# Kernel tuning notes

Measured on AMD Instinct MI355X. Metric: run time of the kernel, lower is better.

Reference implementation:

```python
import jax, jax.numpy as jnp
import numpy as np

H_HEADS = 8
EPS = 1e-5

def layernorm(x, g, b):
    m = jnp.mean(x, axis=-1, keepdims=True)
    v = jnp.mean(jnp.square(x - m), axis=-1, keepdims=True)
    return (x - m) * jax.lax.rsqrt(v + EPS) * g + b

def setup_inputs() -> dict:
    key = jax.random.key(0)
    ks = jax.random.split(key, 8)
    B, H, W, C = 8, 64, 64, 256
    C2 = 2 * C
    s = lambda n: 1.0 / np.sqrt(n)
    return {
        "x1": jax.random.normal(ks[0], (B, H, W, C), jnp.float32),
        "x2": jax.random.normal(ks[1], (B, H, W, C), jnp.float32),
        "norm1_g": jnp.ones((C,)), "norm1_b": jnp.zeros((C,)),
        "lin_w": jax.random.normal(ks[2], (C, C), jnp.float32) * s(C),
        "lin_b": jnp.zeros((C,)),
        "reproj_w": jax.random.normal(ks[3], (C, C), jnp.float32) * s(C),
        "reproj_b": jnp.zeros((C,)),
        "attn_norm_g": jnp.ones((C,)), "attn_norm_b": jnp.zeros((C,)),
        "norm2_g": jnp.ones((C,)), "norm2_b": jnp.zeros((C,)),
        "fc1_w": jax.random.normal(ks[4], (C2, C), jnp.float32) * s(C),
        "fc1_b": jnp.zeros((C2,)),
        "dw_w": jax.random.normal(ks[5], (C2, 1, 3, 3), jnp.float32) * s(9),
        "dw_b": jnp.zeros((C2,)),
        "ffn_n1_g": jnp.ones((C2,)), "ffn_n1_b": jnp.zeros((C2,)),
        "fc2_w": jax.random.normal(ks[6], (C, C2), jnp.float32) * s(C2),
        "fc2_b": jnp.zeros((C,)),
        "ffn_n3_g": jnp.ones((C,)), "ffn_n3_b": jnp.zeros((C,)),
    }

def reference(x1, x2, norm1_g, norm1_b, lin_w, lin_b, reproj_w, reproj_b,
              attn_norm_g, attn_norm_b, norm2_g, norm2_b, fc1_w, fc1_b,
              dw_w, dw_b, ffn_n1_g, ffn_n1_b, fc2_w, fc2_b, ffn_n3_g, ffn_n3_b):
    B, H, W, C = x1.shape
    N = H * W
    h = H_HEADS
    dk = C // h  # head key channels; value_dim == key_dim == C here
    # shared norm1 + linear projection of both streams
    n1 = layernorm(x1, norm1_g, norm1_b) @ lin_w.T + lin_b  # (B,H,W,C) queries src
    n2 = layernorm(x2, norm1_g, norm1_b) @ lin_w.T + lin_b  # (B,H,W,C) key/value src
    # (B,N,C) -> (B,h,d,N); channel dim split contiguously per head (matches torch slicing)
    q = jnp.transpose(n1.reshape(B, N, h, dk), (0, 2, 3, 1))
    k = jnp.transpose(n2.reshape(B, N, h, dk), (0, 2, 3, 1))
    v = k  # values are the same tensor slices (value_dim == key_dim)
    k = jax.nn.softmax(k, axis=-1)   # softmax over tokens N
    q = jax.nn.softmax(q, axis=2)    # softmax over head channel dim
    # linear attention: context (B,h,dk,dv), then project back to tokens
    context = jnp.einsum('bhdn,bhvn->bhdv', k, v)
    att = jnp.einsum('bhdv,bhdn->bhvn', context, q)  # (B,h,dv,N)
    agg = att.reshape(B, C, H, W)
    # 1x1 conv reprojection (value_channels -> key_channels)
    rep = jnp.einsum('bvhw,kv->bhwk', agg, reproj_w) + reproj_b  # (B,H,W,C)
    attn_out = layernorm(rep, attn_norm_g, attn_norm_b)
    # out_proj is Identity since key_dim == in_dim
    tx = attn_out + x1
    y = layernorm(tx, norm2_g, norm2_b)  # skip_ffn input
    # skip_ffn
    h1 = y @ fc1_w.T + fc1_b  # (B,H,W,2C)
    hc = jnp.transpose(h1, (0, 3, 1, 2))  # NCHW
    dw = jax.lax.conv_general_dilated(
        hc, dw_w, window_strides=(1, 1), padding='SAME',
        dimension_numbers=('NCHW', 'OIHW', 'NCHW'),
        feature_group_count=hc.shape[1])
    dw = jnp.transpose(dw + dw_b[None, :, None, None], (0, 2, 3, 1))  # NHWC
    ax = jax.nn.gelu(layernorm(dw, ffn_n1_g, ffn_n1_b), approximate=False)
    out = ax @ fc2_w.T + fc2_b
    return layernorm(out + y, ffn_n3_g, ffn_n3_b)
```

## Files before the change

### kernel.cpp

```cpp
#include <hip/hip_runtime.h>

#define BTOK 32768
#define CC 256
#define CC2 512
#define NBATCH 8

typedef __bf16 bf16x8 __attribute__((ext_vector_type(8)));
typedef float f32x4 __attribute__((ext_vector_type(4)));
typedef unsigned short u16x8 __attribute__((ext_vector_type(8)));
typedef unsigned short u16x4 __attribute__((ext_vector_type(4)));

__device__ __forceinline__ float b2f(unsigned short u) {
    return __uint_as_float(((unsigned)u) << 16);
}
__device__ __forceinline__ unsigned short f2b(float f) {
    unsigned x = __float_as_uint(f);
    return (unsigned short)((x + 0x7fffu + ((x >> 16) & 1u)) >> 16);
}
__device__ __forceinline__ float wredsum(float v) {
#pragma unroll
    for (int m = 1; m < 64; m <<= 1) v += __shfl_xor(v, m);
    return v;
}
__device__ __forceinline__ float grp4sum(float v) {
    v += __shfl_xor(v, 1);
    v += __shfl_xor(v, 2);
    return v;
}

typedef __attribute__((address_space(3))) unsigned int lds_u32;
typedef const __attribute__((address_space(1))) unsigned int glb_u32;
__device__ __forceinline__ void gload_lds16(const unsigned short* g, unsigned short* l) {
    __builtin_amdgcn_global_load_lds((glb_u32*)g, (lds_u32*)l, 16, 0, 0);
}

__global__ __launch_bounds__(256) void probe_kernel(
    const unsigned short* __restrict__ x, int* __restrict__ flag)
{
    int t = threadIdx.x;
    int c = 0;
    for (int i = t; i < 1024; i += 256) {
        unsigned e = (x[i] >> 7) & 0xFFu;
        c += (e >= 110u && e <= 135u) ? 1 : 0;
    }
#pragma unroll
    for (int m = 1; m < 64; m <<= 1) c += __shfl_xor(c, m);
    __shared__ int acc[4];
    if ((t & 63) == 0) acc[t >> 6] = c;
    __syncthreads();
    if (t == 0) *flag = ((acc[0] + acc[1] + acc[2] + acc[3]) >= 896) ? 1 : 0;
}

__global__ __launch_bounds__(256) void cvt_params_kernel(
    const int* __restrict__ flagp,
    const void* p0, const void* p1, const void* p2, const void* p3, const void* p4,
    const void* p5, const void* p6, const void* p7, const void* p8, const void* p9,
    const void* p10, const void* p11, const void* p12, const void* p13, const void* p14,
    const void* p15, const void* p16, const void* p17, const void* p18, const void* p19,
    unsigned short* __restrict__ dst)
{
    bool isb = (*flagp != 0);
    long g = (long)blockIdx.x * 256 + threadIdx.x;
    long str = (long)gridDim.x * 256;
#define CVT(src, off, n)                                                        \
    for (long i = g; i < (long)(n); i += str)                                   \
        dst[(off) + i] = isb ? ((const unsigned short*)(src))[i]                \
                             : f2b(((const float*)(src))[i]);
    CVT(p0, 0, 256)
    CVT(p1, 256, 256)
    CVT(p2, 512, 65536)
    CVT(p3, 66048, 256)
    CVT(p4, 66304, 65536)
    CVT(p5, 131840, 256)
    CVT(p6, 132096, 256)
    CVT(p7, 132352, 256)
    CVT(p8, 132608, 256)
    CVT(p9, 132864, 256)
    CVT(p10, 133120, 131072)
    CVT(p11, 264192, 512)
    CVT(p12, 264704, 4608)
    CVT(p13, 269312, 512)
    CVT(p14, 269824, 512)
    CVT(p15, 270336, 512)
    CVT(p16, 270848, 131072)
    CVT(p17, 401920, 256)
    CVT(p18, 402176, 256)
    CVT(p19, 402432, 256)
#undef CVT
}

__global__ __launch_bounds__(256) void dw_transpose_kernel(
    const void* __restrict__ src, unsigned short* __restrict__ dwt,
    const int* __restrict__ flagp)
{
    bool isb = (*flagp != 0);
    for (int i = threadIdx.x; i < 4608; i += 256) {
        int tap = i >> 9, c = i & 511;
        dwt[i] = isb ? ((const unsigned short*)src)[c * 9 + tap]
                     : f2b(((const float*)src)[c * 9 + tap]);
    }
}

__global__ __launch_bounds__(256) void ln_dual_kernel(
    const void* __restrict__ x1, const void* __restrict__ x2,
    const unsigned short* __restrict__ g, const unsigned short* __restrict__ b,
    unsigned short* __restrict__ out, const int* __restrict__ flagp)
{
    bool isb = (*flagp != 0);
    int wid = threadIdx.x >> 6, l = threadIdx.x & 63;
    long row = (long)blockIdx.x * 4 + wid;
    const void* xsel = (row < BTOK) ? x1 : x2;
    long r = (row < BTOK) ? row : (row - BTOK);
    float f[4];
    if (isb) {
        u16x4 v = *reinterpret_cast<const u16x4*>((const unsigned short*)xsel + r * CC + l * 4);
#pragma unroll
        for (int j = 0; j < 4; j++) f[j] = b2f(v[j]);
    } else {
        f32x4 v = *reinterpret_cast<const f32x4*>((const float*)xsel + r * CC + l * 4);
#pragma unroll
        for (int j = 0; j < 4; j++) f[j] = v[j];
    }
    float mean = wredsum(f[0] + f[1] + f[2] + f[3]) * (1.f / CC);
    float d[4], sq = 0.f;
#pragma unroll
    for (int j = 0; j < 4; j++) { d[j] = f[j] - mean; sq += d[j] * d[j]; }
    float rs = rsqrtf(wredsum(sq) * (1.f / CC) + 1e-5f);
    u16x4 gv = *reinterpret_cast<const u16x4*>(g + l * 4);
    u16x4 bv = *reinterpret_cast<const u16x4*>(b + l * 4);
    u16x4 o;
#pragma unroll
    for (int j = 0; j < 4; j++) o[j] = f2b(d[j] * rs * b2f(gv[j]) + b2f(bv[j]));
    *reinterpret_cast<u16x4*>(out + row * CC + l * 4) = o;
}

template<int K>
__global__ __launch_bounds__(256) void gemm_lds_kernel(
    const unsigned short* __restrict__ A, const unsigned short* __restrict__ Wt,
    const unsigned short* __restrict__ bias, unsigned short* __restrict__ out,
    int O, int nwg)
{
    __shared__ unsigned short Asm[2][4096];
    __shared__ unsigned short Bsm[2][4096];
    int t = threadIdx.x, l = t & 63, w = t >> 6;
    int bid = blockIdx.x, cpx = nwg >> 3;
    int wg = (bid & 7) * cpx + (bid >> 3);
    int ntn = O >> 7;
    long tm = (long)(wg / ntn) << 7;
    int tn = (wg % ntn) << 7;
    int wr = (w >> 1) << 6, wc = (w & 1) << 6;

    int rloc = t >> 2;
    int q = (t & 3) ^ ((t >> 3) & 3);
    const unsigned short* ga0 = A + (tm + rloc) * K + q * 8;
    const unsigned short* ga1 = ga0 + (long)64 * K;
    const unsigned short* gb0 = Wt + (long)(tn + rloc) * K + q * 8;
    const unsigned short* gb1 = gb0 + (long)64 * K;

    int rr = l & 15;
    int sA = ((l >> 4) ^ ((rr >> 1) & 3)) << 3;
    int aoff[4], boff[4];
#pragma unroll
    for (int m = 0; m < 4; m++) aoff[m] = (wr + m * 16 + rr) * 32 + sA;
#pragma unroll
    for (int n = 0; n < 4; n++) boff[n] = (wc + n * 16 + rr) * 32 + sA;

    f32x4 acc[4][4];
#pragma unroll
    for (int m = 0; m < 4; m++)
#pragma unroll
        for (int n = 0; n < 4; n++) acc[m][n] = {0.f, 0.f, 0.f, 0.f};

    auto stage = [&](int buf, int koff) {
        gload_lds16(ga0 + koff, &Asm[buf][w * 512]);
        gload_lds16(ga1 + koff, &Asm[buf][2048 + w * 512]);
        gload_lds16(gb0 + koff, &Bsm[buf][w * 512]);
        gload_lds16(gb1 + koff, &Bsm[buf][2048 + w * 512]);
    };
    auto compute = [&](int buf) {
        bf16x8 af[4], bfr[4];
#pragma unroll
        for (int m = 0; m < 4; m++) af[m] = *reinterpret_cast<const bf16x8*>(&Asm[buf][aoff[m]]);
#pragma unroll
        for (int n = 0; n < 4; n++) bfr[n] = *reinterpret_cast<const bf16x8*>(&Bsm[buf][boff[n]]);
#pragma unroll
        for (int m = 0; m < 4; m++)
#pragma unroll
            for (int n = 0; n < 4; n++)
                acc[m][n] = __builtin_amdgcn_mfma_f32_16x16x32_bf16(af[m], bfr[n], acc[m][n], 0, 0, 0);
    };

    stage(0, 0);
    asm volatile("s_waitcnt vmcnt(0)" ::: "memory");
    __syncthreads();
    constexpr int NK = K / 32;
#pragma unroll
    for (int kt = 0; kt < NK; kt += 2) {
        if (kt + 1 < NK) stage(1, (kt + 1) * 32);
        compute(0);
        asm volatile("s_waitcnt vmcnt(0)" ::: "memory");
        __syncthreads();
        if (kt + 1 < NK) {
            if (kt + 2 < NK) stage(0, (kt + 2) * 32);
            compute(1);
            asm volatile("s_waitcnt vmcnt(0)" ::: "memory");
            __syncthreads();
        }
    }

    int orow = (l >> 4) << 2;
    int ocol = l & 15;
    float bi[4];
#pragma unroll
    for (int n = 0; n < 4; n++) bi[n] = b2f(bias[tn + wc + n * 16 + ocol]);
#pragma unroll
    for (int m = 0; m < 4; m++) {
#pragma unroll
        for (int n = 0; n < 4; n++) {
#pragma unroll
            for (int j = 0; j < 4; j++) {
                out[(tm + wr + m * 16 + orow + j) * O + tn + wc + n * 16 + ocol] =
                    f2b(acc[m][n][j] + bi[n]);
            }
        }
    }
}

#define REPS 272
template<int K, int MODE>
__global__ __launch_bounds__(512) void gemm_fused_kernel(
    const unsigned short* __restrict__ A, const unsigned short* __restrict__ Wt,
    const unsigned short* __restrict__ bias, const void* __restrict__ xin,
    const unsigned short* __restrict__ g1, const unsigned short* __restrict__ b1,
    const unsigned short* __restrict__ g2p, const unsigned short* __restrict__ b2p,
    void* __restrict__ outp, const int* __restrict__ flagp, int nwg)
{
    __shared__ unsigned short SA[2][4096];
    __shared__ unsigned short SB[2][8192];
    __shared__ unsigned short Rep[128 * REPS];
    int t = threadIdx.x, l = t & 63, w = t >> 6;
    int bid = blockIdx.x, cpx = nwg >> 3;
    int wg = (bid & 7) * cpx + (bid >> 3);
    long tm = (long)wg << 7;
    int wr = (w >> 2) << 6, wc = (w & 3) << 6;

    int rloc = t >> 2;
    int q = (t & 3) ^ ((t >> 3) & 3);
    const unsigned short* ga0 = A + (tm + rloc) * K + q * 8;
    const unsigned short* gb0 = Wt + (long)rloc * K + q * 8;
    const unsigned short* gb1 = gb0 + (long)128 * K;

    int rr = l & 15;
    int sA = ((l >> 4) ^ ((rr >> 1) & 3)) << 3;
    int aoff[4], boff[4];
#pragma unroll
    for (int m = 0; m < 4; m++) aoff[m] = (wr + m * 16 + rr) * 32 + sA;
#pragma unroll
    for (int n = 0; n < 4; n++) boff[n] = (wc + n * 16 + rr) * 32 + sA;

    f32x4 acc[4][4];
#pragma unroll
    for (int m = 0; m < 4; m++)
#pragma unroll
        for (int n = 0; n < 4; n++) acc[m][n] = {0.f, 0.f, 0.f, 0.f};

    auto stage = [&](int buf, int koff) {
        gload_lds16(ga0 + koff, &SA[buf][w * 512]);
        gload_lds16(gb0 + koff, &SB[buf][w * 512]);
        gload_lds16(gb1 + koff, &SB[buf][4096 + w * 512]);
    };
    auto compute = [&](int buf) {
        bf16x8 af[4], bfr[4];
#pragma unroll
        for (int m = 0; m < 4; m++) af[m] = *reinterpret_cast<const bf16x8*>(&SA[buf][aoff[m]]);
#pragma unroll
        for (int n = 0; n < 4; n++) bfr[n] = *reinterpret_cast<const bf16x8*>(&SB[buf][boff[n]]);
#pragma unroll
        for (int m = 0; m < 4; m++)
#pragma unroll
            for (int n = 0; n < 4; n++)
                acc[m][n] = __builtin_amdgcn_mfma_f32_16x16x32_bf16(af[m], bfr[n], acc[m][n], 0, 0, 0);
    };

    stage(0, 0);
    asm volatile("s_waitcnt vmcnt(0)" ::: "memory");
    __syncthreads();
    constexpr int NK = K / 32;
#pragma unroll
    for (int kt = 0; kt < NK; kt += 2) {
        if (kt + 1 < NK) stage(1, (kt + 1) * 32);
        compute(0);
        asm volatile("s_waitcnt vmcnt(0)" ::: "memory");
        __syncthreads();
        if (kt + 1 < NK) {
            if (kt + 2 < NK) stage(0, (kt + 2) * 32);
            compute(1);
            asm volatile("s_waitcnt vmcnt(0)" ::: "memory");
            __syncthreads();
        }
    }

    int orow = (l >> 4) << 2, ocol = l & 15;
#pragma unroll
    for (int n = 0; n < 4; n++) {
        float bi = b2f(bias[wc + n * 16 + ocol]);
#pragma unroll
        for (int m = 0; m < 4; m++)
#pragma unroll
            for (int j = 0; j < 4; j++)
                Rep[(wr + m * 16 + orow + j) * REPS + wc + n * 16 + ocol] =
                    f2b(acc[m][n][j] + bi);
    }
    __syncthreads();

    bool isb = (*flagp != 0);
    int r = t >> 2, qd = t & 3;
    long grow = tm + r;
    const unsigned short* rrow = Rep + r * REPS + qd * 8;
    u16x8 rv[8];
#pragma unroll
    for (int i = 0; i < 8; i++) rv[i] = *reinterpret_cast<const u16x8*>(rrow + i * 32);

    if constexpr (MODE == 0) {
        float s1 = 0.f;
#pragma unroll
        for (int i = 0; i < 8; i++)
#pragma unroll
            for (int j = 0; j < 8; j++) s1 += b2f(rv[i][j]);
        s1 = grp4sum(s1);
        float mean = s1 * (1.f / 256);
        float s2 = 0.f;
#pragma unroll
        for (int i = 0; i < 8; i++)
#pragma unroll
            for (int j = 0; j < 8; j++) { float d = b2f(rv[i][j]) - mean; s2 += d * d; }
        s2 = grp4sum(s2);
        float rs = rsqrtf(s2 * (1.f / 256) + 1e-5f);
        const float* xf = (const float*)xin + grow * 256 + qd * 8;
        const unsigned short* xb = (const unsigned short*)xin + grow * 256 + qd * 8;
        float t1 = 0.f, t2 = 0.f;
#pragma unroll
        for (int i = 0; i < 8; i++) {
            int cb = qd * 8 + i * 32;
            u16x8 gg = *reinterpret_cast<const u16x8*>(g1 + cb);
            u16x8 bb = *reinterpret_cast<const u16x8*>(b1 + cb);
            float xv[8];
            if (isb) {
                u16x8 x8 = *reinterpret_cast<const u16x8*>(xb + i * 32);
#pragma unroll
                for (int j = 0; j < 8; j++) xv[j] = b2f(x8[j]);
            } else {
                f32x4 a0 = *reinterpret_cast<const f32x4*>(xf + i * 32);
                f32x4 a1 = *reinterpret_cast<const f32x4*>(xf + i * 32 + 4);
#pragma unroll
                for (int j = 0; j < 4; j++) { xv[j] = a0[j]; xv[4 + j] = a1[j]; }
            }
#pragma unroll
            for (int j = 0; j < 8; j++) {
                float nv = (b2f(rv[i][j]) - mean) * rs * b2f(gg[j]) + b2f(bb[j]);
                float tt = nv + xv[j];
                t1 += tt; t2 += tt * tt;
            }
        }
        t1 = grp4sum(t1); t2 = grp4sum(t2);
        float mean2 = t1 * (1.f / 256);
        float rs2 = rsqrtf(t2 * (1.f / 256) - mean2 * mean2 + 1e-5f);
        unsigned short* ob = (unsigned short*)outp + grow * 256 + qd * 8;
#pragma unroll
        for (int i = 0; i < 8; i++) {
            int cb = qd * 8 + i * 32;
            u16x8 gg = *reinterpret_cast<const u16x8*>(g1 + cb);
            u16x8 bb = *reinterpret_cast<const u16x8*>(b1 + cb);
            u16x8 g2v = *reinterpret_cast<const u16x8*>(g2p + cb);
            u16x8 b2vv = *reinterpret_cast<const u16x8*>(b2p + cb);
            float xv[8];
            if (isb) {
                u16x8 x8 = *reinterpret_cast<const u16x8*>(xb + i * 32);
#pragma unroll
                for (int j = 0; j < 8; j++) xv[j] = b2f(x8[j]);
            } else {
                f32x4 a0 = *reinterpret_cast<const f32x4*>(xf + i * 32);
                f32x4 a1 = *reinterpret_cast<const f32x4*>(xf + i * 32 + 4);
#pragma unroll
                for (int j = 0; j < 4; j++) { xv[j] = a0[j]; xv[4 + j] = a1[j]; }
            }
            u16x8 o;
#pragma unroll
            for (int j = 0; j < 8; j++) {
                float nv = (b2f(rv[i][j]) - mean) * rs * b2f(gg[j]) + b2f(bb[j]);
                float tt = nv + xv[j];
                o[j] = f2b((tt - mean2) * rs2 * b2f(g2v[j]) + b2f(b2vv[j]));
            }
            *reinterpret_cast<u16x8*>(ob + i * 32) = o;
        }
    } else {
        const unsigned short* yb = (const unsigned short*)xin + grow * 256 + qd * 8;
        u16x8 yv[8];
#pragma unroll
        for (int i = 0; i < 8; i++) yv[i] = *reinterpret_cast<const u16x8*>(yb + i * 32);
        float t1 = 0.f, t2 = 0.f;
#pragma unroll
        for (int i = 0; i < 8; i++)
#pragma unroll
            for (int j = 0; j < 8; j++) {
                float tt = b2f(rv[i][j]) + b2f(yv[i][j]);
                t1 += tt; t2 += tt * tt;
            }
        t1 = grp4sum(t1); t2 = grp4sum(t2);
        float mean2 = t1 * (1.f / 256);
        float rs2 = rsqrtf(t2 * (1.f / 256) - mean2 * mean2 + 1e-5f);
        float* of = (float*)outp + grow * 256 + qd * 8;
        unsigned short* ob = (unsigned short*)outp + grow * 256 + qd * 8;
#pragma unroll
        for (int i = 0; i < 8; i++) {
            int cb = qd * 8 + i * 32;
            u16x8 gg = *reinterpret_cast<const u16x8*>(g1 + cb);
            u16x8 bb = *reinterpret_cast<const u16x8*>(b1 + cb);
            float rvals[8];
#pragma unroll
            for (int j = 0; j < 8; j++) {
                float tt = b2f(rv[i][j]) + b2f(yv[i][j]);
                rvals[j] = (tt - mean2) * rs2 * b2f(gg[j]) + b2f(bb[j]);
            }
            if (isb) {
                u16x8 o;
#pragma unroll
                for (int j = 0; j < 8; j++) o[j] = f2b(rvals[j]);
                *reinterpret_cast<u16x8*>(ob + i * 32) = o;
            } else {
                f32x4 o0, o1;
#pragma unroll
                for (int j = 0; j < 4; j++) { o0[j] = rvals[j]; o1[j] = rvals[4 + j]; }
                *reinterpret_cast<f32x4*>(of + i * 32) = o0;
                *reinterpret_cast<f32x4*>(of + i * 32 + 4) = o1;
            }
        }
    }
}

__global__ __launch_bounds__(256) void colstats1_kernel(
    const unsigned short* __restrict__ n2, float* __restrict__ pm, float* __restrict__ ps)
{
    int b = blockIdx.x >> 6, slab = blockIdx.x & 63;
    int t = threadIdx.x;
    int c0 = (t & 63) << 2;
    int r = t >> 6;
    const unsigned short* base = n2 + ((long)b * 4096 + slab * 64 + r) * CC + c0;
    float m[4] = {-3.0e38f, -3.0e38f, -3.0e38f, -3.0e38f};
    float s[4] = {0.f, 0.f, 0.f, 0.f};
#pragma unroll 4
    for (int i = 0; i < 16; i++) {
        u16x4 v = *reinterpret_cast<const u16x4*>(base + (long)i * 4 * CC);
#pragma unroll
        for (int j = 0; j < 4; j++) {
            float x = b2f(v[j]);
            if (x > m[j]) { s[j] = s[j] * __expf(m[j] - x) + 1.f; m[j] = x; }
            else s[j] += __expf(x - m[j]);
        }
    }
    __shared__ float lm[4][256], lsb[4][256];
#pragma unroll
    for (int j = 0; j < 4; j++) { lm[r][c0 + j] = m[j]; lsb[r][c0 + j] = s[j]; }
    __syncthreads();
    if (r == 0) {
#pragma unroll
        for (int w = 1; w < 4; w++) {
#pragma unroll
            for (int j = 0; j < 4; j++) {
                float mi = lm[w][c0 + j], si = lsb[w][c0 + j];
                if (mi > m[j]) { s[j] = s[j] * __expf(m[j] - mi) + si; m[j] = mi; }
                else s[j] += si * __expf(mi - m[j]);
            }
        }
        long o = ((long)(b * 64 + slab)) * 256 + c0;
#pragma unroll
        for (int j = 0; j < 4; j++) { pm[o + j] = m[j]; ps[o + j] = s[j]; }
    }
}

__global__ __launch_bounds__(256) void colstats2_kernel(
    const float* __restrict__ pm, const float* __restrict__ ps,
    float* __restrict__ kmax, float* __restrict__ ksum)
{
    int b = blockIdx.x, c = threadIdx.x;
    float M = -3.0e38f, S = 0.f;
    for (int s = 0; s < 64; s++) {
        long o = ((long)(b * 64 + s)) * 256 + c;
        float mi = pm[o], si = ps[o];
        if (mi > M) { S = S * __expf(M - mi) + si; M = mi; }
        else S += si * __expf(mi - M);
    }
    kmax[b * CC + c] = M;
    ksum[b * CC + c] = S;
}

__global__ __launch_bounds__(256) void ctx_part_kernel(
    const unsigned short* __restrict__ n2, const float* __restrict__ kmax,
    const float* __restrict__ ksum, float* __restrict__ pctx)
{
    int blk = blockIdx.x;
    int b = blk >> 7, hd = (blk >> 4) & 7, slab = blk & 15;
    int t = threadIdx.x;
    __shared__ float ld[32][33], eld[32][33];
    int d = t >> 3;
    int v0 = (t & 7) << 2;
    int ln_ = t >> 3;
    int lc = (t & 7) << 2;
    float kmx4[4], kin4[4];
#pragma unroll
    for (int j = 0; j < 4; j++) {
        kmx4[j] = kmax[b * CC + hd * 32 + lc + j];
        kin4[j] = 1.f / ksum[b * CC + hd * 32 + lc + j];
    }
    f32x4 acc = {0.f, 0.f, 0.f, 0.f};
    const unsigned short* base = n2 + ((long)b * 4096 + slab * 256) * CC + hd * 32;
    for (int n0 = 0; n0 < 256; n0 += 32) {
        u16x4 rv = *reinterpret_cast<const u16x4*>(base + (long)(n0 + ln_) * CC + lc);
#pragma unroll
        for (int j = 0; j < 4; j++) {
            float x = b2f(rv[j]);
            ld[ln_][lc + j] = x;
            eld[ln_][lc + j] = __expf(x - kmx4[j]) * kin4[j];
        }
        __syncthreads();
#pragma unroll 4
        for (int nn = 0; nn < 32; nn++) {
            float e = eld[nn][d];
#pragma unroll
            for (int j = 0; j < 4; j++) acc[j] += e * ld[nn][v0 + j];
        }
        __syncthreads();
    }
    long o = ((long)slab * NBATCH * 8 + (long)b * 8 + hd) * 1024 + (long)d * 32 + v0;
#pragma unroll
    for (int j = 0; j < 4; j++) pctx[o + j] = acc[j];
}

__global__ __launch_bounds__(256) void ctx_reduce_kernel(
    const float* __restrict__ pctx, float* __restrict__ ctx)
{
    long i = (long)blockIdx.x * 256 + threadIdx.x;
    float s = 0.f;
#pragma unroll
    for (int sl = 0; sl < 16; sl++) s += pctx[(long)sl * 65536 + i];
    ctx[i] = s;
}

__global__ __launch_bounds__(256) void att_kernel(
    const unsigned short* __restrict__ n1, const float* __restrict__ ctx,
    unsigned short* __restrict__ attv)
{
    __shared__ float cl[32 * 256];
    __shared__ float ql[4][264];
    int b = blockIdx.x >> 6, grp = blockIdx.x & 63;
    int t = threadIdx.x, wid = t >> 6, l = t & 63;
    const float* cb = ctx + (long)b * 8192;
    for (int i = 0; i < 32; i++) {
        int gidx = t + (i << 8);
        int hd_ = gidx >> 10, dd = (gidx >> 5) & 31, vv = gidx & 31;
        cl[dd * 256 + hd_ * 32 + vv] = cb[gidx];
    }
    __syncthreads();
    int hd = l >> 3;
    long tokbase = (long)b * 4096 + grp * 64 + wid * 16;
    const f32x4* c4 = reinterpret_cast<const f32x4*>(cl);
    for (int it = 0; it < 16; it++) {
        long tok = tokbase + it;
        u16x4 rv = *reinterpret_cast<const u16x4*>(n1 + tok * CC + l * 4);
        float x[4];
#pragma unroll
        for (int j = 0; j < 4; j++) x[j] = b2f(rv[j]);
        float mx = fmaxf(fmaxf(x[0], x[1]), fmaxf(x[2], x[3]));
        mx = fmaxf(mx, __shfl_xor(mx, 1));
        mx = fmaxf(mx, __shfl_xor(mx, 2));
        mx = fmaxf(mx, __shfl_xor(mx, 4));
        float e[4], s = 0.f;
#pragma unroll
        for (int j = 0; j < 4; j++) { e[j] = __expf(x[j] - mx); s += e[j]; }
        s += __shfl_xor(s, 1);
        s += __shfl_xor(s, 2);
        s += __shfl_xor(s, 4);
        float inv = 1.f / s;
#pragma unroll
        for (int j = 0; j < 4; j++) ql[wid][hd * 33 + ((l & 7) << 2) + j] = e[j] * inv;
        __syncthreads();
        f32x4 o = {0.f, 0.f, 0.f, 0.f};
#pragma unroll 8
        for (int dd = 0; dd < 32; dd++) {
            float qd = ql[wid][hd * 33 + dd];
            o += qd * c4[dd * 64 + l];
        }
        __syncthreads();
        u16x4 ov;
#pragma unroll
        for (int j = 0; j < 4; j++) ov[j] = f2b(o[j]);
        *reinterpret_cast<u16x4*>(attv + tok * CC + l * 4) = ov;
    }
}

__global__ __launch_bounds__(256) void dw_kernel(
    const unsigned short* __restrict__ h1, const unsigned short* __restrict__ dwt,
    const unsigned short* __restrict__ dwb, const unsigned short* __restrict__ g,
    const unsigned short* __restrict__ bb, unsigned short* __restrict__ ax)
{
    int wid = threadIdx.x >> 6, l = threadIdx.x & 63;
    int pix = blockIdx.x * 4 + wid;
    int b = pix >> 12, rem = pix & 4095, py = rem >> 6, px = rem & 63;
    int c0 = l * 8;
    u16x8 wv[9];
#pragma unroll
    for (int tap = 0; tap < 9; tap++)
        wv[tap] = *reinterpret_cast<const u16x8*>(dwt + tap * CC2 + c0);
    u16x8 biasv = *reinterpret_cast<const u16x8*>(dwb + c0);
    float acc[8];
#pragma unroll
    for (int j = 0; j < 8; j++) acc[j] = b2f(biasv[j]);
#pragma unroll
    for (int ky = 0; ky < 3; ky++) {
        int ys = py + ky - 1;
        if ((unsigned)ys >= 64u) continue;
#pragma unroll
        for (int kx = 0; kx < 3; kx++) {
            int xs = px + kx - 1;
            if ((unsigned)xs >= 64u) continue;
            u16x8 pv = *reinterpret_cast<const u16x8*>(
                h1 + ((long)(b << 12) + (ys << 6) + xs) * CC2 + c0);
            int tap = ky * 3 + kx;
#pragma unroll
            for (int j = 0; j < 8; j++)
                acc[j] += b2f(pv[j]) * b2f(wv[tap][j]);
        }
    }
    float s = 0.f;
#pragma unroll
    for (int j = 0; j < 8; j++) s += acc[j];
    float mean = wredsum(s) * (1.f / CC2);
    float d[8], sq = 0.f;
#pragma unroll
    for (int j = 0; j < 8; j++) { d[j] = acc[j] - mean; sq += d[j] * d[j]; }
    float rs = rsqrtf(wredsum(sq) * (1.f / CC2) + 1e-5f);
    u16x8 gv = *reinterpret_cast<const u16x8*>(g + c0);
    u16x8 bv = *reinterpret_cast<const u16x8*>(bb + c0);
    u16x8 o;
#pragma unroll
    for (int j = 0; j < 8; j++) {
        float nv = d[j] * rs * b2f(gv[j]) + b2f(bv[j]);
        o[j] = f2b(0.5f * nv * (1.f + erff(nv * 0.70710678118654752f)));
    }
    *reinterpret_cast<u16x8*>(ax + (long)pix * CC2 + c0) = o;
}

extern "C" void kernel_launch(void* const* d_in, const int* in_sizes, int n_in,
                              void* d_out, int out_size, void* d_ws, size_t ws_size,
                              hipStream_t stream)
{
    char* w = (char*)d_ws;
    const size_t S1B = (size_t)BTOK * CC * 2;
    const size_t STATSB = (size_t)(2 * NBATCH * CC + NBATCH * 8 * 32 * 32) * 4;
    const size_t PARAMS_ELEMS = 402688 + 4608;
    const size_t need = 6 * S1B + STATSB + 64 + PARAMS_ELEMS * 2;
    if (ws_size < need) return;

    unsigned short* ln12 = (unsigned short*)w;
    unsigned short* n12  = (unsigned short*)(w + 2 * S1B);
    unsigned short* nn1  = n12;
    unsigned short* nn2  = n12 + (size_t)BTOK * CC;
    unsigned short* attv = ln12;
    unsigned short* ybuf = nn1;
    unsigned short* h1   = ln12;
    unsigned short* axb  = (unsigned short*)(w + 4 * S1B);
    float* pm   = (float*)(w + 4 * S1B);
    float* ps   = (float*)(w + 4 * S1B + (512 << 10));
    float* pctx = (float*)(w + 4 * S1B + (2048 << 10));
    float* kmax = (float*)(w + 6 * S1B);
    float* ksum = kmax + NBATCH * CC;
    float* ctxb = ksum + NBATCH * CC;
    int*   flag = (int*)(w + 6 * S1B + STATSB);
    unsigned short* pb = (unsigned short*)(w + 6 * S1B + STATSB + 64);

    unsigned short* n1g  = pb + 0;
    unsigned short* n1b  = pb + 256;
    unsigned short* linw = pb + 512;
    unsigned short* linb = pb + 66048;
    unsigned short* repw = pb + 66304;
    unsigned short* repb = pb + 131840;
    unsigned short* ang  = pb + 132096;
    unsigned short* anb  = pb + 132352;
    unsigned short* g2   = pb + 132608;
    unsigned short* b2v  = pb + 132864;
    unsigned short* fc1w = pb + 133120;
    unsigned short* fc1b = pb + 264192;
    unsigned short* dwb  = pb + 269312;
    unsigned short* fn1g = pb + 269824;
    unsigned short* fn1b = pb + 270336;
    unsigned short* fc2w = pb + 270848;
    unsigned short* fc2b = pb + 401920;
    unsigned short* fn3g = pb + 402176;
    unsigned short* fn3b = pb + 402432;
    unsigned short* dwt  = pb + 402688;

    probe_kernel<<<1, 256, 0, stream>>>((const unsigned short*)d_in[0], flag);
    cvt_params_kernel<<<512, 256, 0, stream>>>(flag,
        d_in[2], d_in[3], d_in[4], d_in[5], d_in[6], d_in[7], d_in[8], d_in[9],
        d_in[10], d_in[11], d_in[12], d_in[13], d_in[14], d_in[15], d_in[16],
        d_in[17], d_in[18], d_in[19], d_in[20], d_in[21], pb);
    dw_transpose_kernel<<<1, 256, 0, stream>>>(d_in[14], dwt, flag);
    ln_dual_kernel<<<2 * BTOK / 4, 256, 0, stream>>>(d_in[0], d_in[1], n1g, n1b, ln12, flag);
    {
        int nwg = (2 * BTOK / 128) * (CC / 128);
        gemm_lds_kernel<256><<<nwg, 256, 0, stream>>>(ln12, linw, linb, n12, CC, nwg);
    }
    colstats1_kernel<<<NBATCH * 64, 256, 0, stream>>>(nn2, pm, ps);
    colstats2_kernel<<<NBATCH, 256, 0, stream>>>(pm, ps, kmax, ksum);
    ctx_part_kernel<<<NBATCH * 8 * 16, 256, 0, stream>>>(nn2, kmax, ksum, pctx);
    ctx_reduce_kernel<<<256, 256, 0, stream>>>(pctx, ctxb);
    att_kernel<<<NBATCH * 64, 256, 0, stream>>>(nn1, ctxb, attv);
    {
        int nwg = BTOK / 128;
        gemm_fused_kernel<256, 0><<<nwg, 512, 0, stream>>>(
            attv, repw, repb, d_in[0], ang, anb, g2, b2v, ybuf, flag, nwg);
    }
    {
        int nwg = (BTOK / 128) * (CC2 / 128);
        gemm_lds_kernel<256><<<nwg, 256, 0, stream>>>(ybuf, fc1w, fc1b, h1, CC2, nwg);
    }
    dw_kernel<<<BTOK / 4, 256, 0, stream>>>(h1, dwt, dwb, fn1g, fn1b, axb);
    {
        int nwg = BTOK / 128;
        gemm_fused_kernel<512, 1><<<nwg, 512, 0, stream>>>(
            axb, fc2w, fc2b, ybuf, fn3g, fn3b, fn3g, fn3b, d_out, flag, nwg);
    }
}
```

Baseline: 233.2 us.

## Fold key softmax normalization into context reduce, drop column-stats kernels

Removes the two column-statistics kernels by computing unnormalized exp(k) in the context partial kernel, accumulating per-channel exp sums alongside it, and dividing by those sums in the reduce step. This saves a full pass over the key tensor and two launches. The exp is no longer max-shifted, which risks overflow for large activations. It also keeps the fused residual layernorm values in registers instead of reloading x and params, and replaces the LDS staging plus barriers in the attention kernel with lane shuffles, scaling by the inverse sum at the end.

```diff
diff --git a/kernel.cpp b/kernel.cpp
--- a/kernel.cpp
+++ b/kernel.cpp
@@ -338,6 +338,7 @@
         float rs = rsqrtf(s2 * (1.f / 256) + 1e-5f);
         const float* xf = (const float*)xin + grow * 256 + qd * 8;
         const unsigned short* xb = (const unsigned short*)xin + grow * 256 + qd * 8;
+        float tt[8][8];
         float t1 = 0.f, t2 = 0.f;
 #pragma unroll
         for (int i = 0; i < 8; i++) {
@@ -358,8 +359,9 @@
 #pragma unroll
             for (int j = 0; j < 8; j++) {
                 float nv = (b2f(rv[i][j]) - mean) * rs * b2f(gg[j]) + b2f(bb[j]);
-                float tt = nv + xv[j];
-                t1 += tt; t2 += tt * tt;
+                float v = nv + xv[j];
+                tt[i][j] = v;
+                t1 += v; t2 += v * v;
             }
         }
         t1 = grp4sum(t1); t2 = grp4sum(t2);
@@ -369,28 +371,12 @@
 #pragma unroll
         for (int i = 0; i < 8; i++) {
             int cb = qd * 8 + i * 32;
-            u16x8 gg = *reinterpret_cast<const u16x8*>(g1 + cb);
-            u16x8 bb = *reinterpret_cast<const u16x8*>(b1 + cb);
             u16x8 g2v = *reinterpret_cast<const u16x8*>(g2p + cb);
             u16x8 b2vv = *reinterpret_cast<const u16x8*>(b2p + cb);
-            float xv[8];
-            if (isb) {
-                u16x8 x8 = *reinterpret_cast<const u16x8*>(xb + i * 32);
-#pragma unroll
-                for (int j = 0; j < 8; j++) xv[j] = b2f(x8[j]);
-            } else {
-                f32x4 a0 = *reinterpret_cast<const f32x4*>(xf + i * 32);
-                f32x4 a1 = *reinterpret_cast<const f32x4*>(xf + i * 32 + 4);
-#pragma unroll
-                for (int j = 0; j < 4; j++) { xv[j] = a0[j]; xv[4 + j] = a1[j]; }
-            }
             u16x8 o;
 #pragma unroll
-            for (int j = 0; j < 8; j++) {
-                float nv = (b2f(rv[i][j]) - mean) * rs * b2f(gg[j]) + b2f(bb[j]);
-                float tt = nv + xv[j];
-                o[j] = f2b((tt - mean2) * rs2 * b2f(g2v[j]) + b2f(b2vv[j]));
-            }
+            for (int j = 0; j < 8; j++)
+                o[j] = f2b((tt[i][j] - mean2) * rs2 * b2f(g2v[j]) + b2f(b2vv[j]));
             *reinterpret_cast<u16x8*>(ob + i * 32) = o;
         }
     } else {
@@ -438,65 +424,9 @@
     }
 }
 
-__global__ __launch_bounds__(256) void colstats1_kernel(
-    const unsigned short* __restrict__ n2, float* __restrict__ pm, float* __restrict__ ps)
-{
-    int b = blockIdx.x >> 6, slab = blockIdx.x & 63;
-    int t = threadIdx.x;
-    int c0 = (t & 63) << 2;
-    int r = t >> 6;
-    const unsigned short* base = n2 + ((long)b * 4096 + slab * 64 + r) * CC + c0;
-    float m[4] = {-3.0e38f, -3.0e38f, -3.0e38f, -3.0e38f};
-    float s[4] = {0.f, 0.f, 0.f, 0.f};
-#pragma unroll 4
-    for (int i = 0; i < 16; i++) {
-        u16x4 v = *reinterpret_cast<const u16x4*>(base + (long)i * 4 * CC);
-#pragma unroll
-        for (int j = 0; j < 4; j++) {
-            float x = b2f(v[j]);
-            if (x > m[j]) { s[j] = s[j] * __expf(m[j] - x) + 1.f; m[j] = x; }
-            else s[j] += __expf(x - m[j]);
-        }
-    }
-    __shared__ float lm[4][256], lsb[4][256];
-#pragma unroll
-    for (int j = 0; j < 4; j++) { lm[r][c0 + j] = m[j]; lsb[r][c0 + j] = s[j]; }
-    __syncthreads();
-    if (r == 0) {
-#pragma unroll
-        for (int w = 1; w < 4; w++) {
-#pragma unroll
-            for (int j = 0; j < 4; j++) {
-                float mi = lm[w][c0 + j], si = lsb[w][c0 + j];
-                if (mi > m[j]) { s[j] = s[j] * __expf(m[j] - mi) + si; m[j] = mi; }
-                else s[j] += si * __expf(mi - m[j]);
-            }
-        }
-        long o = ((long)(b * 64 + slab)) * 256 + c0;
-#pragma unroll
-        for (int j = 0; j < 4; j++) { pm[o + j] = m[j]; ps[o + j] = s[j]; }
-    }
-}
-
-__global__ __launch_bounds__(256) void colstats2_kernel(
-    const float* __restrict__ pm, const float* __restrict__ ps,
-    float* __restrict__ kmax, float* __restrict__ ksum)
-{
-    int b = blockIdx.x, c = threadIdx.x;
-    float M = -3.0e38f, S = 0.f;
-    for (int s = 0; s < 64; s++) {
-        long o = ((long)(b * 64 + s)) * 256 + c;
-        float mi = pm[o], si = ps[o];
-        if (mi > M) { S = S * __expf(M - mi) + si; M = mi; }
-        else S += si * __expf(mi - M);
-    }
-    kmax[b * CC + c] = M;
-    ksum[b * CC + c] = S;
-}
-
 __global__ __launch_bounds__(256) void ctx_part_kernel(
-    const unsigned short* __restrict__ n2, const float* __restrict__ kmax,
-    const float* __restrict__ ksum, float* __restrict__ pctx)
+    const unsigned short* __restrict__ n2, float* __restrict__ pctx,
+    float* __restrict__ pcs)
 {
     int blk = blockIdx.x;
     int b = blk >> 7, hd = (blk >> 4) & 7, slab = blk & 15;
@@ -506,13 +436,8 @@
     int v0 = (t & 7) << 2;
     int ln_ = t >> 3;
     int lc = (t & 7) << 2;
-    float kmx4[4], kin4[4];
-#pragma unroll
-    for (int j = 0; j < 4; j++) {
-        kmx4[j] = kmax[b * CC + hd * 32 + lc + j];
-        kin4[j] = 1.f / ksum[b * CC + hd * 32 + lc + j];
-    }
     f32x4 acc = {0.f, 0.f, 0.f, 0.f};
+    float se = 0.f;
     const unsigned short* base = n2 + ((long)b * 4096 + slab * 256) * CC + hd * 32;
     for (int n0 = 0; n0 < 256; n0 += 32) {
         u16x4 rv = *reinterpret_cast<const u16x4*>(base + (long)(n0 + ln_) * CC + lc);
@@ -520,12 +445,13 @@
         for (int j = 0; j < 4; j++) {
             float x = b2f(rv[j]);
             ld[ln_][lc + j] = x;
-            eld[ln_][lc + j] = __expf(x - kmx4[j]) * kin4[j];
+            eld[ln_][lc + j] = __expf(x);
         }
         __syncthreads();
 #pragma unroll 4
         for (int nn = 0; nn < 32; nn++) {
             float e = eld[nn][d];
+            se += e;
 #pragma unroll
             for (int j = 0; j < 4; j++) acc[j] += e * ld[nn][v0 + j];
         }
@@ -534,16 +460,24 @@
     long o = ((long)slab * NBATCH * 8 + (long)b * 8 + hd) * 1024 + (long)d * 32 + v0;
 #pragma unroll
     for (int j = 0; j < 4; j++) pctx[o + j] = acc[j];
+    if ((t & 7) == 0)
+        pcs[(long)slab * (NBATCH * 8 * 32) + ((long)(b * 8 + hd) << 5) + d] = se;
 }
 
 __global__ __launch_bounds__(256) void ctx_reduce_kernel(
-    const float* __restrict__ pctx, float* __restrict__ ctx)
+    const float* __restrict__ pctx, const float* __restrict__ pcs,
+    float* __restrict__ ctx)
 {
     long i = (long)blockIdx.x * 256 + threadIdx.x;
-    float s = 0.f;
-#pragma unroll
-    for (int sl = 0; sl < 16; sl++) s += pctx[(long)sl * 65536 + i];
-    ctx[i] = s;
+    int bh = (int)(i >> 10);
+    int d = (int)((i >> 5) & 31);
+    float s = 0.f, ps = 0.f;
+#pragma unroll
+    for (int sl = 0; sl < 16; sl++) {
+        s += pctx[(long)sl * 65536 + i];
+        ps += pcs[(long)sl * (NBATCH * 8 * 32) + (bh << 5) + d];
+    }
+    ctx[i] = s / ps;
 }
 
 __global__ __launch_bounds__(256) void att_kernel(
@@ -551,7 +485,6 @@
     unsigned short* __restrict__ attv)
 {
     __shared__ float cl[32 * 256];
-    __shared__ float ql[4][264];
     int b = blockIdx.x >> 6, grp = blockIdx.x & 63;
     int t = threadIdx.x, wid = t >> 6, l = t & 63;
     const float* cb = ctx + (long)b * 8192;
@@ -561,7 +494,7 @@
         cl[dd * 256 + hd_ * 32 + vv] = cb[gidx];
     }
     __syncthreads();
-    int hd = l >> 3;
+    int base_lane = l & 56;
     long tokbase = (long)b * 4096 + grp * 64 + wid * 16;
     const f32x4* c4 = reinterpret_cast<const f32x4*>(cl);
     for (int it = 0; it < 16; it++) {
@@ -581,16 +514,13 @@
         s += __shfl_xor(s, 2);
         s += __shfl_xor(s, 4);
         float inv = 1.f / s;
-#pragma unroll
-        for (int j = 0; j < 4; j++) ql[wid][hd * 33 + ((l & 7) << 2) + j] = e[j] * inv;
-        __syncthreads();
         f32x4 o = {0.f, 0.f, 0.f, 0.f};
-#pragma unroll 8
+#pragma unroll
         for (int dd = 0; dd < 32; dd++) {
-            float qd = ql[wid][hd * 33 + dd];
-            o += qd * c4[dd * 64 + l];
-        }
-        __syncthreads();
+            float qv = __shfl(e[dd & 3], base_lane + (dd >> 2));
+            o += qv * c4[dd * 64 + l];
+        }
+        o *= inv;
         u16x4 ov;
 #pragma unroll
         for (int j = 0; j < 4; j++) ov[j] = f2b(o[j]);
@@ -669,12 +599,9 @@
     unsigned short* ybuf = nn1;
     unsigned short* h1   = ln12;
     unsigned short* axb  = (unsigned short*)(w + 4 * S1B);
-    float* pm   = (float*)(w + 4 * S1B);
-    float* ps   = (float*)(w + 4 * S1B + (512 << 10));
     float* pctx = (float*)(w + 4 * S1B + (2048 << 10));
-    float* kmax = (float*)(w + 6 * S1B);
-    float* ksum = kmax + NBATCH * CC;
-    float* ctxb = ksum + NBATCH * CC;
+    float* pcs  = (float*)(w + 4 * S1B + (2048 << 10) + (4 << 20));
+    float* ctxb = (float*)(w + 6 * S1B) + 2 * NBATCH * CC;
     int*   flag = (int*)(w + 6 * S1B + STATSB);
     unsigned short* pb = (unsigned short*)(w + 6 * S1B + STATSB + 64);
 
@@ -710,10 +637,8 @@
         int nwg = (2 * BTOK / 128) * (CC / 128);
         gemm_lds_kernel<256><<<nwg, 256, 0, stream>>>(ln12, linw, linb, n12, CC, nwg);
     }
-    colstats1_kernel<<<NBATCH * 64, 256, 0, stream>>>(nn2, pm, ps);
-    colstats2_kernel<<<NBATCH, 256, 0, stream>>>(pm, ps, kmax, ksum);
-    ctx_part_kernel<<<NBATCH * 8 * 16, 256, 0, stream>>>(nn2, kmax, ksum, pctx);
-    ctx_reduce_kernel<<<256, 256, 0, stream>>>(pctx, ctxb);
+    ctx_part_kernel<<<NBATCH * 8 * 16, 256, 0, stream>>>(nn2, pctx, pcs);
+    ctx_reduce_kernel<<<256, 256, 0, stream>>>(pctx, pcs, ctxb);
     att_kernel<<<NBATCH * 64, 256, 0, stream>>>(nn1, ctxb, attv);
     {
         int nwg = BTOK / 128;
```

Result: faster. 204.7 us (-12.2%).
